# Kernel optimization log

Measured on AMD Instinct MI355X. Metric: run time of the kernel, lower is better.

Reference implementation:

```python
import jax, jax.numpy as jnp
import numpy as np

NUM_BITS = 10
MEM_SIZE = 2 ** NUM_BITS  # 1024
HIDDEN = 1024
INPUT = 1024
BATCH = 16384
LN_EPS = 1e-5


def setup_inputs() -> dict:
    key = jax.random.key(0)
    ks = jax.random.split(key, 8)
    s = 0.02
    return {
        "x": jax.random.normal(ks[0], (BATCH, INPUT), jnp.float32),
        "h_prev": jax.random.normal(ks[1], (BATCH, HIDDEN), jnp.float32),
        "memory": jax.random.normal(ks[2], (MEM_SIZE, HIDDEN), jnp.float32),
        "W_w": jax.random.normal(ks[3], (HIDDEN, INPUT), jnp.float32) * s,
        "W_b": jnp.zeros((HIDDEN,), jnp.float32),
        "U_w": jax.random.normal(ks[4], (HIDDEN, HIDDEN), jnp.float32) * s,
        "U_b": jnp.zeros((HIDDEN,), jnp.float32),
        "Q_w": jax.random.normal(ks[5], (HIDDEN, HIDDEN), jnp.float32) * s,
        "Q_b": jnp.zeros((HIDDEN,), jnp.float32),
        "M_w": jax.random.normal(ks[6], (NUM_BITS, HIDDEN), jnp.float32) * s,
        "M_b": jnp.zeros((NUM_BITS,), jnp.float32),
        "ln_g": jnp.ones((HIDDEN,), jnp.float32),
        "ln_b": jnp.zeros((HIDDEN,), jnp.float32),
    }


def reference(x, h_prev, memory, W_w, W_b, U_w, U_b, Q_w, Q_b, M_w, M_b, ln_g, ln_b):
    # Binary address from h_prev (eval-mode hard threshold, non-differentiable)
    powers = jnp.asarray(2 ** np.arange(NUM_BITS - 1, -1, -1), dtype=x.dtype)  # [num_bits]
    logits = h_prev @ M_w.T + M_b                              # [B, num_bits]
    binary = (jax.nn.sigmoid(logits) > 0.5).astype(x.dtype)    # hard bits
    index = jnp.clip((binary * powers).sum(-1).astype(jnp.int32), 0, MEM_SIZE - 1)  # [B]
    h_mem = memory[index]                                      # gather [B, H]
    # Fused linear combine + LayerNorm + sigmoid
    pre = x @ W_w.T + W_b + h_prev @ U_w.T + U_b + h_mem @ Q_w.T + Q_b  # [B, H]
    mu = pre.mean(-1, keepdims=True)
    var = ((pre - mu) ** 2).mean(-1, keepdims=True)            # biased var (torch LN)
    norm = (pre - mu) * jax.lax.rsqrt(var + LN_EPS)
    return jax.nn.sigmoid(norm * ln_g + ln_b)                  # h_new [B, H]
```

## Files before the change

### kernel.cpp

```cpp
#include <hip/hip_runtime.h>

#define BATCH   16384
#define HIDDEN  1024
#define K2      2048
#define MEMSZ   1024
#define NBITS   10

#define BM 256
#define BN 256
#define BK 64
#define NT (K2 / BK)

#define U_BM    262144
#define U_TOT   2359296
#define SBLK    2304
#define SSTRIDE (SBLK * 256)

typedef __bf16 bf16x8 __attribute__((ext_vector_type(8)));
typedef float  f32x4  __attribute__((ext_vector_type(4)));
typedef unsigned short u16x8 __attribute__((ext_vector_type(8)));

__device__ __forceinline__ unsigned short f2bf(float f) {
    unsigned int u = __float_as_uint(f);
    u += 0x7FFFu + ((u >> 16) & 1u);
    return (unsigned short)(u >> 16);
}

__device__ __forceinline__ float bf2f(unsigned short u) {
    return __uint_as_float((unsigned int)u << 16);
}

__device__ __forceinline__ u16x8 f2bf8(float4 a, float4 b) {
    u16x8 r;
    r[0] = f2bf(a.x); r[1] = f2bf(a.y); r[2] = f2bf(a.z); r[3] = f2bf(a.w);
    r[4] = f2bf(b.x); r[5] = f2bf(b.y); r[6] = f2bf(b.z); r[7] = f2bf(b.w);
    return r;
}

__device__ __forceinline__ ushort4 f2bf4(float4 a) {
    ushort4 r;
    r.x = f2bf(a.x); r.y = f2bf(a.y); r.z = f2bf(a.z); r.w = f2bf(a.w);
    return r;
}

__device__ __forceinline__ void gload_lds16(const void* g, void* l) {
    __builtin_amdgcn_global_load_lds(
        (const __attribute__((address_space(1))) unsigned int*)g,
        (__attribute__((address_space(3))) unsigned int*)l,
        16, 0, 0);
}

__global__ __launch_bounds__(256) void stream_kernel(
        const float* __restrict__ W, const float* __restrict__ U,
        const float* __restrict__ x,
        unsigned short* __restrict__ Bm, unsigned short* __restrict__ A) {
    const int u0 = blockIdx.x * 256 + threadIdx.x;
    const float* s4[4];
    unsigned short* d4[4];
#pragma unroll
    for (int i = 0; i < 4; ++i) {
        int u = u0 + i * SSTRIDE;
        if (u < U_BM) {
            int n  = u >> 8;
            int k8 = (u & 255) << 3;
            s4[i] = (k8 < 1024) ? (W + (size_t)n * 1024 + k8)
                                : (U + (size_t)n * 1024 + (k8 - 1024));
            d4[i] = Bm + (size_t)n * K2 + k8;
        } else {
            int e = (u - U_BM) << 3;
            int row = e >> 10, col = e & 1023;
            s4[i] = x + (size_t)row * HIDDEN + col;
            d4[i] = A + (size_t)row * K2 + col;
        }
    }
    float4 va[4], vb[4];
#pragma unroll
    for (int i = 0; i < 4; ++i) {
        va[i] = *reinterpret_cast<const float4*>(s4[i]);
        vb[i] = *reinterpret_cast<const float4*>(s4[i] + 4);
    }
    __builtin_amdgcn_sched_barrier(0);
#pragma unroll
    for (int i = 0; i < 4; ++i)
        *reinterpret_cast<u16x8*>(d4[i]) = f2bf8(va[i], vb[i]);
}

__global__ __launch_bounds__(256) void build_kernel(
        const float* __restrict__ h_prev,
        const float* __restrict__ M_w, const float* __restrict__ M_b,
        unsigned short* __restrict__ A, int* __restrict__ idxbuf) {
    __shared__ float mw[NBITS * HIDDEN];
    for (int i = threadIdx.x; i < (NBITS * HIDDEN) / 4; i += 256)
        reinterpret_cast<float4*>(mw)[i] = reinterpret_cast<const float4*>(M_w)[i];
    __syncthreads();

    const int wv   = threadIdx.x >> 6;
    const int lane = threadIdx.x & 63;
    const int row0 = (blockIdx.x * 4 + wv) * 2;
    const int c4   = lane * 4;

    float4 h[2][4];
#pragma unroll
    for (int r = 0; r < 2; ++r) {
        const float* hr = h_prev + (size_t)(row0 + r) * HIDDEN;
#pragma unroll
        for (int seg = 0; seg < 4; ++seg)
            h[r][seg] = *reinterpret_cast<const float4*>(hr + seg * 256 + c4);
    }

    float s[2][NBITS];
#pragma unroll
    for (int j = 0; j < NBITS; ++j) {
        const float* mj = mw + j * HIDDEN;
        float4 m[4];
#pragma unroll
        for (int seg = 0; seg < 4; ++seg)
            m[seg] = *reinterpret_cast<const float4*>(mj + seg * 256 + c4);
#pragma unroll
        for (int r = 0; r < 2; ++r) {
            float acc = 0.f;
#pragma unroll
            for (int seg = 0; seg < 4; ++seg)
                acc += h[r][seg].x * m[seg].x + h[r][seg].y * m[seg].y
                     + h[r][seg].z * m[seg].z + h[r][seg].w * m[seg].w;
            s[r][j] = acc;
        }
    }
#pragma unroll
    for (int off = 32; off >= 1; off >>= 1) {
#pragma unroll
        for (int r = 0; r < 2; ++r)
#pragma unroll
            for (int j = 0; j < NBITS; ++j)
                s[r][j] += __shfl_xor(s[r][j], off, 64);
    }
#pragma unroll
    for (int r = 0; r < 2; ++r) {
        int idx = 0;
#pragma unroll
        for (int j = 0; j < NBITS; ++j)
            if (s[r][j] + M_b[j] > 0.f) idx |= 1 << (NBITS - 1 - j);
        if (lane == 0) idxbuf[row0 + r] = idx;
    }

#pragma unroll
    for (int r = 0; r < 2; ++r) {
        unsigned short* arow = A + (size_t)(row0 + r) * K2 + 1024;
#pragma unroll
        for (int seg = 0; seg < 4; ++seg)
            *reinterpret_cast<ushort4*>(arow + seg * 256 + c4) = f2bf4(h[r][seg]);
    }
}

__global__ __launch_bounds__(256) void mq_kernel(
        const float* __restrict__ memory,
        const float* __restrict__ Q,
        float* __restrict__ MQ) {
    __shared__ unsigned short As[128 * 32];
    __shared__ unsigned short Bs[128 * 32];

    const int mb = blockIdx.x >> 3;
    const int nb = blockIdx.x & 7;
    const int t    = threadIdx.x;
    const int lane = t & 63;
    const int w    = t >> 6;
    const int wr   = w >> 1, wc = w & 1;
    const int rr   = lane & 15, rq = lane >> 4;
    const int srow = t >> 1;
    const int scol = (t & 1) * 16;
    const int swr  = (srow & 3) << 4;

    f32x4 acc[4][4] = {};

    for (int kt = 0; kt < 32; ++kt) {
        const int k0 = kt * 32;
        const float* ap = memory + (size_t)(mb * 128 + srow) * 1024 + k0 + scol;
        const float* bp = Q      + (size_t)(nb * 128 + srow) * 1024 + k0 + scol;
        float4 a0 = *reinterpret_cast<const float4*>(ap);
        float4 a1 = *reinterpret_cast<const float4*>(ap + 4);
        float4 a2 = *reinterpret_cast<const float4*>(ap + 8);
        float4 a3 = *reinterpret_cast<const float4*>(ap + 12);
        float4 b0 = *reinterpret_cast<const float4*>(bp);
        float4 b1 = *reinterpret_cast<const float4*>(bp + 4);
        float4 b2 = *reinterpret_cast<const float4*>(bp + 8);
        float4 b3 = *reinterpret_cast<const float4*>(bp + 12);
        __syncthreads();
        {
            char* ar = reinterpret_cast<char*>(As) + srow * 64;
            char* br = reinterpret_cast<char*>(Bs) + srow * 64;
            *reinterpret_cast<u16x8*>(ar + ((scol * 2)      ^ swr)) = f2bf8(a0, a1);
            *reinterpret_cast<u16x8*>(ar + ((scol * 2 + 16) ^ swr)) = f2bf8(a2, a3);
            *reinterpret_cast<u16x8*>(br + ((scol * 2)      ^ swr)) = f2bf8(b0, b1);
            *reinterpret_cast<u16x8*>(br + ((scol * 2 + 16) ^ swr)) = f2bf8(b2, b3);
        }
        __syncthreads();
        bf16x8 af[4], bfv[4];
#pragma unroll
        for (int m = 0; m < 4; ++m) {
            int r = wr * 64 + m * 16 + rr;
            af[m] = *reinterpret_cast<const bf16x8*>(
                reinterpret_cast<const char*>(As) + r * 64 + ((rq * 16) ^ ((r & 3) << 4)));
        }
#pragma unroll
        for (int n = 0; n < 4; ++n) {
            int r = wc * 64 + n * 16 + rr;
            bfv[n] = *reinterpret_cast<const bf16x8*>(
                reinterpret_cast<const char*>(Bs) + r * 64 + ((rq * 16) ^ ((r & 3) << 4)));
        }
#pragma unroll
        for (int m = 0; m < 4; ++m)
#pragma unroll
            for (int n = 0; n < 4; ++n)
                acc[m][n] = __builtin_amdgcn_mfma_f32_16x16x32_bf16(
                    af[m], bfv[n], acc[m][n], 0, 0, 0);
    }

#pragma unroll
    for (int m = 0; m < 4; ++m)
#pragma unroll
        for (int n = 0; n < 4; ++n) {
            int gcol = nb * 128 + wc * 64 + n * 16 + rr;
#pragma unroll
            for (int j = 0; j < 4; ++j) {
                int grow = mb * 128 + wr * 64 + m * 16 + rq * 4 + j;
                MQ[(size_t)grow * 1024 + gcol] = acc[m][n][j];
            }
        }
}


__device__ __forceinline__ void stage_g(const unsigned short* __restrict__ src,
                                        int rowbase, int kt, int g,
                                        unsigned short* ldsTile, int t) {
    const int o      = g * 8192 + t * 16;
    const int row    = o >> 7;
    const int inner  = o & 127;
    const int sinner = inner ^ ((row & 7) << 4);
    const char* gp = reinterpret_cast<const char*>(
                         src + (size_t)(rowbase + row) * K2 + kt * BK) + sinner;
    gload_lds16(gp, reinterpret_cast<char*>(ldsTile) + o);
}

__device__ __forceinline__ bf16x8 ldsfrag(const unsigned short* tile, int row,
                                          int kbyte_x_sw) {
    return *reinterpret_cast<const bf16x8*>(
        reinterpret_cast<const char*>(tile) + row * 128 + kbyte_x_sw);
}

#define PH_BAR()                                                     \
    do {                                                             \
        asm volatile("" ::: "memory");                               \
        __builtin_amdgcn_s_barrier();                                \
        asm volatile("" ::: "memory");                               \
    } while (0)

#define LGKM(N)                                                      \
    do {                                                             \
        asm volatile("s_waitcnt lgkmcnt(" #N ")" ::: "memory");      \
        __builtin_amdgcn_sched_barrier(0);                           \
    } while (0)

#define MFMA_Q(AF, BF, MB, NB)                                                 \
    {                                                                          \
        __builtin_amdgcn_s_setprio(1);                                         \
        _Pragma("unroll") for (int m_ = 0; m_ < 4; ++m_)                       \
        _Pragma("unroll") for (int n_ = 0; n_ < 2; ++n_)                       \
        _Pragma("unroll") for (int kk_ = 0; kk_ < 2; ++kk_)                    \
            acc[(MB) + m_][(NB) + n_] =                                        \
                __builtin_amdgcn_mfma_f32_16x16x32_bf16(                       \
                    AF[m_][kk_], BF[n_][kk_],                                  \
                    acc[(MB) + m_][(NB) + n_], 0, 0, 0);                       \
        __builtin_amdgcn_s_setprio(0);                                         \
    }

template <bool BF16C>
__global__ __launch_bounds__(512, 2) void gemm_kernel(
        const unsigned short* __restrict__ A,
        const unsigned short* __restrict__ Bm,
        void* __restrict__ Cout) {
    __shared__ alignas(16) unsigned short lds[2][2][BM * BK];

    const int bid  = blockIdx.x;
    const int wgid = (bid & 7) * 32 + (bid >> 3);
    const int mblk = wgid >> 2;
    const int nblk = wgid & 3;

    const int t    = threadIdx.x;
    const int lane = t & 63;
    const int w    = t >> 6;
    const int wr   = w >> 2;
    const int wc   = w & 3;
    const int rr   = lane & 15;
    const int rq   = lane >> 4;
    const int sw   = (rr & 7) << 4;
    const int rqb  = rq * 16;
    const int wrb  = wr * 128;
    const int wcb  = wc * 64;

    const int arow = mblk * BM;
    const int brow = nblk * BN;

    f32x4 acc[8][4] = {};

    {
#pragma unroll
        for (int g = 0; g < 4; ++g) stage_g(A,  arow, 0, g, &lds[0][0][0], t);
#pragma unroll
        for (int g = 0; g < 4; ++g) stage_g(Bm, brow, 0, g, &lds[0][1][0], t);
#pragma unroll
        for (int g = 0; g < 4; ++g) stage_g(Bm, brow, 1, g, &lds[1][1][0], t);
#pragma unroll
        for (int g = 0; g < 4; ++g) stage_g(A,  arow, 1, g, &lds[1][0][0], t);
        asm volatile("s_waitcnt vmcnt(8)" ::: "memory");
        asm volatile("" ::: "memory");
        __builtin_amdgcn_s_barrier();
    }

    bf16x8 af  [4][2];
    bf16x8 af2 [4][2];
    bf16x8 bfr01[2][2];
    bf16x8 bfr23[2][2];

#pragma unroll
    for (int m = 0; m < 4; ++m) {
        af[m][0] = ldsfrag(&lds[0][0][0], wrb + m * 16 + rr, (rqb) ^ sw);
        af[m][1] = ldsfrag(&lds[0][0][0], wrb + m * 16 + rr, (64 + rqb) ^ sw);
    }
#pragma unroll
    for (int n = 0; n < 2; ++n) {
        bfr01[n][0] = ldsfrag(&lds[0][1][0], wcb + n * 16 + rr, (rqb) ^ sw);
        bfr01[n][1] = ldsfrag(&lds[0][1][0], wcb + n * 16 + rr, (64 + rqb) ^ sw);
    }

    for (int kt = 0; kt < NT; ++kt) {
        const int c = kt & 1;
        const unsigned short* At  = &lds[c][0][0];
        const unsigned short* Bt  = &lds[c][1][0];
        const unsigned short* nxA = &lds[c ^ 1][0][0];
        const unsigned short* nxB = &lds[c ^ 1][1][0];
        unsigned short* curA = &lds[c][0][0];
        unsigned short* curB = &lds[c][1][0];
        const bool pf1 = (kt + 1 < NT);
        const bool pf2 = (kt + 2 < NT);

        PH_BAR();
#pragma unroll
        for (int n = 0; n < 2; ++n) {
            bfr23[n][0] = ldsfrag(Bt, wcb + 32 + n * 16 + rr, (rqb) ^ sw);
            bfr23[n][1] = ldsfrag(Bt, wcb + 32 + n * 16 + rr, (64 + rqb) ^ sw);
        }
        af2[0][0] = ldsfrag(At, wrb + 64 + rr, (rqb) ^ sw);
        af2[0][1] = ldsfrag(At, wrb + 64 + rr, (64 + rqb) ^ sw);
        LGKM(6);
        MFMA_Q(af, bfr01, 0, 0);

        PH_BAR();
#pragma unroll
        for (int m = 1; m < 4; ++m) {
            af2[m][0] = ldsfrag(At, wrb + 64 + m * 16 + rr, (rqb) ^ sw);
            af2[m][1] = ldsfrag(At, wrb + 64 + m * 16 + rr, (64 + rqb) ^ sw);
        }
        LGKM(8);
        MFMA_Q(af, bfr23, 0, 2);
        __builtin_amdgcn_sched_barrier(0);
        asm volatile("s_waitcnt vmcnt(0)" ::: "memory");
        asm volatile("" ::: "memory");

        PH_BAR();
        if (pf2) {
            stage_g(Bm, brow, kt + 2, 0, curB, t);
            stage_g(Bm, brow, kt + 2, 1, curB, t);
            stage_g(Bm, brow, kt + 2, 2, curB, t);
            stage_g(Bm, brow, kt + 2, 3, curB, t);
        }
        if (pf1) {
#pragma unroll
            for (int m = 0; m < 3; ++m) {
                af[m][0] = ldsfrag(nxA, wrb + m * 16 + rr, (rqb) ^ sw);
                af[m][1] = ldsfrag(nxA, wrb + m * 16 + rr, (64 + rqb) ^ sw);
            }
            LGKM(6);
        } else {
            LGKM(0);
        }
        MFMA_Q(af2, bfr01, 4, 0);

        PH_BAR();
        if (pf2) {
            stage_g(A, arow, kt + 2, 0, curA, t);
            stage_g(A, arow, kt + 2, 1, curA, t);
            stage_g(A, arow, kt + 2, 2, curA, t);
            stage_g(A, arow, kt + 2, 3, curA, t);
        }
        if (pf1) {
            af[3][0] = ldsfrag(nxA, wrb + 48 + rr, (rqb) ^ sw);
            af[3][1] = ldsfrag(nxA, wrb + 48 + rr, (64 + rqb) ^ sw);
#pragma unroll
            for (int n = 0; n < 2; ++n) {
                bfr01[n][0] = ldsfrag(nxB, wcb + n * 16 + rr, (rqb) ^ sw);
                bfr01[n][1] = ldsfrag(nxB, wcb + n * 16 + rr, (64 + rqb) ^ sw);
            }
        }
        MFMA_Q(af2, bfr23, 4, 2);
    }

#pragma unroll
    for (int mi = 0; mi < 8; ++mi) {
#pragma unroll
        for (int n = 0; n < 4; ++n) {
            const int gcol = nblk * BN + wcb + n * 16 + rr;
#pragma unroll
            for (int j = 0; j < 4; ++j) {
                const int grow = mblk * BM + wrb + mi * 16 + rq * 4 + j;
                if constexpr (BF16C) {
                    ((unsigned short*)Cout)[(size_t)grow * HIDDEN + gcol] =
                        f2bf(acc[mi][n][j]);
                } else {
                    ((float*)Cout)[(size_t)grow * HIDDEN + gcol] = acc[mi][n][j];
                }
            }
        }
    }
}

template <bool BF16C>
__global__ __launch_bounds__(256) void ln_kernel(
        const void* __restrict__ Cin, float* __restrict__ out,
        const int* __restrict__ idxbuf,
        const float* __restrict__ MQ,
        const float* __restrict__ W_b, const float* __restrict__ U_b,
        const float* __restrict__ Q_b, const float* __restrict__ ln_g,
        const float* __restrict__ ln_b) {
    const int row = blockIdx.x;
    const int t   = threadIdx.x;
    const int midx = idxbuf[row];
    const float4* mqp = reinterpret_cast<const float4*>(MQ + (size_t)midx * HIDDEN);

    float4 p;
    if constexpr (BF16C) {
        ushort4 uv = reinterpret_cast<const ushort4*>(
            (const unsigned short*)Cin + (size_t)row * HIDDEN)[t];
        p.x = bf2f(uv.x); p.y = bf2f(uv.y); p.z = bf2f(uv.z); p.w = bf2f(uv.w);
    } else {
        p = reinterpret_cast<const float4*>(
            (const float*)Cin + (size_t)row * HIDDEN)[t];
    }
    float4 mq = mqp[t];
    float4 bw = reinterpret_cast<const float4*>(W_b)[t];
    float4 bu = reinterpret_cast<const float4*>(U_b)[t];
    float4 bq = reinterpret_cast<const float4*>(Q_b)[t];
    p.x += mq.x + bw.x + bu.x + bq.x;
    p.y += mq.y + bw.y + bu.y + bq.y;
    p.z += mq.z + bw.z + bu.z + bq.z;
    p.w += mq.w + bw.w + bu.w + bq.w;

    float s  = p.x + p.y + p.z + p.w;
    float sq = p.x * p.x + p.y * p.y + p.z * p.z + p.w * p.w;
#pragma unroll
    for (int off = 32; off >= 1; off >>= 1) {
        s  += __shfl_xor(s,  off, 64);
        sq += __shfl_xor(sq, off, 64);
    }
    __shared__ float red[8];
    const int lane = t & 63, w = t >> 6;
    if (lane == 0) { red[w] = s; red[4 + w] = sq; }
    __syncthreads();
    const float S    = red[0] + red[1] + red[2] + red[3];
    const float SQ   = red[4] + red[5] + red[6] + red[7];
    const float mean = S * (1.0f / HIDDEN);
    const float var  = SQ * (1.0f / HIDDEN) - mean * mean;
    const float rstd = rsqrtf(var + 1e-5f);

    float4 g = reinterpret_cast<const float4*>(ln_g)[t];
    float4 b = reinterpret_cast<const float4*>(ln_b)[t];
    float4 o;
    o.x = 1.f / (1.f + __expf(-((p.x - mean) * rstd * g.x + b.x)));
    o.y = 1.f / (1.f + __expf(-((p.y - mean) * rstd * g.y + b.y)));
    o.z = 1.f / (1.f + __expf(-((p.z - mean) * rstd * g.z + b.z)));
    o.w = 1.f / (1.f + __expf(-((p.w - mean) * rstd * g.w + b.w)));
    reinterpret_cast<float4*>(out + (size_t)row * HIDDEN)[t] = o;
}

extern "C" void kernel_launch(void* const* d_in, const int* in_sizes, int n_in,
                              void* d_out, int out_size, void* d_ws, size_t ws_size,
                              hipStream_t stream) {
    const float* x      = (const float*)d_in[0];
    const float* h_prev = (const float*)d_in[1];
    const float* memory = (const float*)d_in[2];
    const float* W_w    = (const float*)d_in[3];
    const float* W_b    = (const float*)d_in[4];
    const float* U_w    = (const float*)d_in[5];
    const float* U_b    = (const float*)d_in[6];
    const float* Q_w    = (const float*)d_in[7];
    const float* Q_b    = (const float*)d_in[8];
    const float* M_w    = (const float*)d_in[9];
    const float* M_b    = (const float*)d_in[10];
    const float* ln_g   = (const float*)d_in[11];
    const float* ln_b   = (const float*)d_in[12];

    char* ws = (char*)d_ws;
    unsigned short* A   = (unsigned short*)(ws);
    unsigned short* Bm  = (unsigned short*)(ws + 67108864);
    float*          MQ  = (float*)         (ws + 71303168);
    int*            idx = (int*)           (ws + 75497472);
    unsigned short* Cb  = (unsigned short*)(ws + 75563008);
    const bool bf16c = ws_size >= (size_t)75563008 + 33554432;

    float* pre = (float*)d_out;

    hipLaunchKernelGGL(stream_kernel, dim3(SBLK), dim3(256), 0, stream,
                       W_w, U_w, x, Bm, A);
    hipLaunchKernelGGL(build_kernel, dim3(BATCH / 8), dim3(256), 0, stream,
                       h_prev, M_w, M_b, A, idx);
    hipLaunchKernelGGL(mq_kernel, dim3(64), dim3(256), 0, stream,
                       memory, Q_w, MQ);
    if (bf16c) {
        hipLaunchKernelGGL((gemm_kernel<true>), dim3((BATCH / BM) * (HIDDEN / BN)),
                           dim3(512), 0, stream, A, Bm, (void*)Cb);
        hipLaunchKernelGGL((ln_kernel<true>), dim3(BATCH), dim3(256), 0, stream,
                           (const void*)Cb, (float*)d_out, idx, MQ,
                           W_b, U_b, Q_b, ln_g, ln_b);
    } else {
        hipLaunchKernelGGL((gemm_kernel<false>), dim3((BATCH / BM) * (HIDDEN / BN)),
                           dim3(512), 0, stream, A, Bm, (void*)pre);
        hipLaunchKernelGGL((ln_kernel<false>), dim3(BATCH), dim3(256), 0, stream,
                           (const void*)pre, (float*)d_out, idx, MQ,
                           W_b, U_b, Q_b, ln_g, ln_b);
    }
}
```

Baseline: 187.1 us.

## Merge front-end kernels into one launch and drop bf16 intermediate path

```diff
diff --git a/kernel.cpp b/kernel.cpp
--- a/kernel.cpp
+++ b/kernel.cpp
@@ -11,10 +11,12 @@
 #define BK 64
 #define NT (K2 / BK)
 
+#define MQB     64
 #define U_BM    262144
 #define U_TOT   2359296
 #define SBLK    2304
 #define SSTRIDE (SBLK * 256)
+#define BBLK    (BATCH / 8)
 
 typedef __bf16 bf16x8 __attribute__((ext_vector_type(8)));
 typedef float  f32x4  __attribute__((ext_vector_type(4)));
@@ -24,10 +26,6 @@
     unsigned int u = __float_as_uint(f);
     u += 0x7FFFu + ((u >> 16) & 1u);
     return (unsigned short)(u >> 16);
-}
-
-__device__ __forceinline__ float bf2f(unsigned short u) {
-    return __uint_as_float((unsigned int)u << 16);
 }
 
 __device__ __forceinline__ u16x8 f2bf8(float4 a, float4 b) {
@@ -50,53 +48,130 @@
         16, 0, 0);
 }
 
-__global__ __launch_bounds__(256) void stream_kernel(
+__global__ __launch_bounds__(256) void front_kernel(
         const float* __restrict__ W, const float* __restrict__ U,
-        const float* __restrict__ x,
-        unsigned short* __restrict__ Bm, unsigned short* __restrict__ A) {
-    const int u0 = blockIdx.x * 256 + threadIdx.x;
-    const float* s4[4];
-    unsigned short* d4[4];
-#pragma unroll
-    for (int i = 0; i < 4; ++i) {
-        int u = u0 + i * SSTRIDE;
-        if (u < U_BM) {
-            int n  = u >> 8;
-            int k8 = (u & 255) << 3;
-            s4[i] = (k8 < 1024) ? (W + (size_t)n * 1024 + k8)
-                                : (U + (size_t)n * 1024 + (k8 - 1024));
-            d4[i] = Bm + (size_t)n * K2 + k8;
-        } else {
-            int e = (u - U_BM) << 3;
-            int row = e >> 10, col = e & 1023;
-            s4[i] = x + (size_t)row * HIDDEN + col;
-            d4[i] = A + (size_t)row * K2 + col;
-        }
-    }
-    float4 va[4], vb[4];
-#pragma unroll
-    for (int i = 0; i < 4; ++i) {
-        va[i] = *reinterpret_cast<const float4*>(s4[i]);
-        vb[i] = *reinterpret_cast<const float4*>(s4[i] + 4);
-    }
-    __builtin_amdgcn_sched_barrier(0);
-#pragma unroll
-    for (int i = 0; i < 4; ++i)
-        *reinterpret_cast<u16x8*>(d4[i]) = f2bf8(va[i], vb[i]);
-}
-
-__global__ __launch_bounds__(256) void build_kernel(
-        const float* __restrict__ h_prev,
+        const float* __restrict__ x, const float* __restrict__ h_prev,
+        const float* __restrict__ memory, const float* __restrict__ Q,
         const float* __restrict__ M_w, const float* __restrict__ M_b,
-        unsigned short* __restrict__ A, int* __restrict__ idxbuf) {
-    __shared__ float mw[NBITS * HIDDEN];
+        unsigned short* __restrict__ Bm, unsigned short* __restrict__ A,
+        float* __restrict__ MQ, int* __restrict__ idxbuf) {
+    __shared__ alignas(16) char shmem[40960];
+
+    if (blockIdx.x < MQB) {
+        unsigned short* As = reinterpret_cast<unsigned short*>(shmem);
+        unsigned short* Bs = reinterpret_cast<unsigned short*>(shmem + 8192);
+
+        const int mb = blockIdx.x >> 3;
+        const int nb = blockIdx.x & 7;
+        const int t    = threadIdx.x;
+        const int lane = t & 63;
+        const int w    = t >> 6;
+        const int wr   = w >> 1, wc = w & 1;
+        const int rr   = lane & 15, rq = lane >> 4;
+        const int srow = t >> 1;
+        const int scol = (t & 1) * 16;
+        const int swr  = (srow & 3) << 4;
+
+        f32x4 acc[4][4] = {};
+
+        for (int kt = 0; kt < 32; ++kt) {
+            const int k0 = kt * 32;
+            const float* ap = memory + (size_t)(mb * 128 + srow) * 1024 + k0 + scol;
+            const float* bp = Q      + (size_t)(nb * 128 + srow) * 1024 + k0 + scol;
+            float4 a0 = *reinterpret_cast<const float4*>(ap);
+            float4 a1 = *reinterpret_cast<const float4*>(ap + 4);
+            float4 a2 = *reinterpret_cast<const float4*>(ap + 8);
+            float4 a3 = *reinterpret_cast<const float4*>(ap + 12);
+            float4 b0 = *reinterpret_cast<const float4*>(bp);
+            float4 b1 = *reinterpret_cast<const float4*>(bp + 4);
+            float4 b2 = *reinterpret_cast<const float4*>(bp + 8);
+            float4 b3 = *reinterpret_cast<const float4*>(bp + 12);
+            __syncthreads();
+            {
+                char* ar = reinterpret_cast<char*>(As) + srow * 64;
+                char* br = reinterpret_cast<char*>(Bs) + srow * 64;
+                *reinterpret_cast<u16x8*>(ar + ((scol * 2)      ^ swr)) = f2bf8(a0, a1);
+                *reinterpret_cast<u16x8*>(ar + ((scol * 2 + 16) ^ swr)) = f2bf8(a2, a3);
+                *reinterpret_cast<u16x8*>(br + ((scol * 2)      ^ swr)) = f2bf8(b0, b1);
+                *reinterpret_cast<u16x8*>(br + ((scol * 2 + 16) ^ swr)) = f2bf8(b2, b3);
+            }
+            __syncthreads();
+            bf16x8 af[4], bfv[4];
+#pragma unroll
+            for (int m = 0; m < 4; ++m) {
+                int r = wr * 64 + m * 16 + rr;
+                af[m] = *reinterpret_cast<const bf16x8*>(
+                    reinterpret_cast<const char*>(As) + r * 64 + ((rq * 16) ^ ((r & 3) << 4)));
+            }
+#pragma unroll
+            for (int n = 0; n < 4; ++n) {
+                int r = wc * 64 + n * 16 + rr;
+                bfv[n] = *reinterpret_cast<const bf16x8*>(
+                    reinterpret_cast<const char*>(Bs) + r * 64 + ((rq * 16) ^ ((r & 3) << 4)));
+            }
+#pragma unroll
+            for (int m = 0; m < 4; ++m)
+#pragma unroll
+                for (int n = 0; n < 4; ++n)
+                    acc[m][n] = __builtin_amdgcn_mfma_f32_16x16x32_bf16(
+                        af[m], bfv[n], acc[m][n], 0, 0, 0);
+        }
+
+#pragma unroll
+        for (int m = 0; m < 4; ++m)
+#pragma unroll
+            for (int n = 0; n < 4; ++n) {
+                int gcol = nb * 128 + wc * 64 + n * 16 + rr;
+#pragma unroll
+                for (int j = 0; j < 4; ++j) {
+                    int grow = mb * 128 + wr * 64 + m * 16 + rq * 4 + j;
+                    MQ[(size_t)grow * 1024 + gcol] = acc[m][n][j];
+                }
+            }
+        return;
+    }
+
+    if (blockIdx.x < MQB + SBLK) {
+        const int u0 = (blockIdx.x - MQB) * 256 + threadIdx.x;
+        const float* s4[4];
+        unsigned short* d4[4];
+#pragma unroll
+        for (int i = 0; i < 4; ++i) {
+            int u = u0 + i * SSTRIDE;
+            if (u < U_BM) {
+                int n  = u >> 8;
+                int k8 = (u & 255) << 3;
+                s4[i] = (k8 < 1024) ? (W + (size_t)n * 1024 + k8)
+                                    : (U + (size_t)n * 1024 + (k8 - 1024));
+                d4[i] = Bm + (size_t)n * K2 + k8;
+            } else {
+                int e = (u - U_BM) << 3;
+                int row = e >> 10, col = e & 1023;
+                s4[i] = x + (size_t)row * HIDDEN + col;
+                d4[i] = A + (size_t)row * K2 + col;
+            }
+        }
+        float4 va[4], vb[4];
+#pragma unroll
+        for (int i = 0; i < 4; ++i) {
+            va[i] = *reinterpret_cast<const float4*>(s4[i]);
+            vb[i] = *reinterpret_cast<const float4*>(s4[i] + 4);
+        }
+        __builtin_amdgcn_sched_barrier(0);
+#pragma unroll
+        for (int i = 0; i < 4; ++i)
+            *reinterpret_cast<u16x8*>(d4[i]) = f2bf8(va[i], vb[i]);
+        return;
+    }
+
+    float* mw = reinterpret_cast<float*>(shmem);
     for (int i = threadIdx.x; i < (NBITS * HIDDEN) / 4; i += 256)
         reinterpret_cast<float4*>(mw)[i] = reinterpret_cast<const float4*>(M_w)[i];
     __syncthreads();
 
     const int wv   = threadIdx.x >> 6;
     const int lane = threadIdx.x & 63;
-    const int row0 = (blockIdx.x * 4 + wv) * 2;
+    const int row0 = ((blockIdx.x - MQB - SBLK) * 4 + wv) * 2;
     const int c4   = lane * 4;
 
     float4 h[2][4];
@@ -150,82 +225,6 @@
         for (int seg = 0; seg < 4; ++seg)
             *reinterpret_cast<ushort4*>(arow + seg * 256 + c4) = f2bf4(h[r][seg]);
     }
-}
-
-__global__ __launch_bounds__(256) void mq_kernel(
-        const float* __restrict__ memory,
-        const float* __restrict__ Q,
-        float* __restrict__ MQ) {
-    __shared__ unsigned short As[128 * 32];
-    __shared__ unsigned short Bs[128 * 32];
-
-    const int mb = blockIdx.x >> 3;
-    const int nb = blockIdx.x & 7;
-    const int t    = threadIdx.x;
-    const int lane = t & 63;
-    const int w    = t >> 6;
-    const int wr   = w >> 1, wc = w & 1;
-    const int rr   = lane & 15, rq = lane >> 4;
-    const int srow = t >> 1;
-    const int scol = (t & 1) * 16;
-    const int swr  = (srow & 3) << 4;
-
-    f32x4 acc[4][4] = {};
-
-    for (int kt = 0; kt < 32; ++kt) {
-        const int k0 = kt * 32;
-        const float* ap = memory + (size_t)(mb * 128 + srow) * 1024 + k0 + scol;
-        const float* bp = Q      + (size_t)(nb * 128 + srow) * 1024 + k0 + scol;
-        float4 a0 = *reinterpret_cast<const float4*>(ap);
-        float4 a1 = *reinterpret_cast<const float4*>(ap + 4);
-        float4 a2 = *reinterpret_cast<const float4*>(ap + 8);
-        float4 a3 = *reinterpret_cast<const float4*>(ap + 12);
-        float4 b0 = *reinterpret_cast<const float4*>(bp);
-        float4 b1 = *reinterpret_cast<const float4*>(bp + 4);
-        float4 b2 = *reinterpret_cast<const float4*>(bp + 8);
-        float4 b3 = *reinterpret_cast<const float4*>(bp + 12);
-        __syncthreads();
-        {
-            char* ar = reinterpret_cast<char*>(As) + srow * 64;
-            char* br = reinterpret_cast<char*>(Bs) + srow * 64;
-            *reinterpret_cast<u16x8*>(ar + ((scol * 2)      ^ swr)) = f2bf8(a0, a1);
-            *reinterpret_cast<u16x8*>(ar + ((scol * 2 + 16) ^ swr)) = f2bf8(a2, a3);
-            *reinterpret_cast<u16x8*>(br + ((scol * 2)      ^ swr)) = f2bf8(b0, b1);
-            *reinterpret_cast<u16x8*>(br + ((scol * 2 + 16) ^ swr)) = f2bf8(b2, b3);
-        }
-        __syncthreads();
-        bf16x8 af[4], bfv[4];
-#pragma unroll
-        for (int m = 0; m < 4; ++m) {
-            int r = wr * 64 + m * 16 + rr;
-            af[m] = *reinterpret_cast<const bf16x8*>(
-                reinterpret_cast<const char*>(As) + r * 64 + ((rq * 16) ^ ((r & 3) << 4)));
-        }
-#pragma unroll
-        for (int n = 0; n < 4; ++n) {
-            int r = wc * 64 + n * 16 + rr;
-            bfv[n] = *reinterpret_cast<const bf16x8*>(
-                reinterpret_cast<const char*>(Bs) + r * 64 + ((rq * 16) ^ ((r & 3) << 4)));
-        }
-#pragma unroll
-        for (int m = 0; m < 4; ++m)
-#pragma unroll
-            for (int n = 0; n < 4; ++n)
-                acc[m][n] = __builtin_amdgcn_mfma_f32_16x16x32_bf16(
-                    af[m], bfv[n], acc[m][n], 0, 0, 0);
-    }
-
-#pragma unroll
-    for (int m = 0; m < 4; ++m)
-#pragma unroll
-        for (int n = 0; n < 4; ++n) {
-            int gcol = nb * 128 + wc * 64 + n * 16 + rr;
-#pragma unroll
-            for (int j = 0; j < 4; ++j) {
-                int grow = mb * 128 + wr * 64 + m * 16 + rq * 4 + j;
-                MQ[(size_t)grow * 1024 + gcol] = acc[m][n][j];
-            }
-        }
 }
 
 
@@ -273,11 +272,10 @@
         __builtin_amdgcn_s_setprio(0);                                         \
     }
 
-template <bool BF16C>
 __global__ __launch_bounds__(512, 2) void gemm_kernel(
         const unsigned short* __restrict__ A,
         const unsigned short* __restrict__ Bm,
-        void* __restrict__ Cout) {
+        float* __restrict__ C) {
     __shared__ alignas(16) unsigned short lds[2][2][BM * BK];
 
     const int bid  = blockIdx.x;
@@ -412,20 +410,14 @@
 #pragma unroll
             for (int j = 0; j < 4; ++j) {
                 const int grow = mblk * BM + wrb + mi * 16 + rq * 4 + j;
-                if constexpr (BF16C) {
-                    ((unsigned short*)Cout)[(size_t)grow * HIDDEN + gcol] =
-                        f2bf(acc[mi][n][j]);
-                } else {
-                    ((float*)Cout)[(size_t)grow * HIDDEN + gcol] = acc[mi][n][j];
-                }
-            }
-        }
-    }
-}
-
-template <bool BF16C>
+                C[(size_t)grow * HIDDEN + gcol] = acc[mi][n][j];
+            }
+        }
+    }
+}
+
 __global__ __launch_bounds__(256) void ln_kernel(
-        const void* __restrict__ Cin, float* __restrict__ out,
+        float* __restrict__ C,
         const int* __restrict__ idxbuf,
         const float* __restrict__ MQ,
         const float* __restrict__ W_b, const float* __restrict__ U_b,
@@ -434,17 +426,10 @@
     const int row = blockIdx.x;
     const int t   = threadIdx.x;
     const int midx = idxbuf[row];
+    float4* rowp = reinterpret_cast<float4*>(C + (size_t)row * HIDDEN);
     const float4* mqp = reinterpret_cast<const float4*>(MQ + (size_t)midx * HIDDEN);
 
-    float4 p;
-    if constexpr (BF16C) {
-        ushort4 uv = reinterpret_cast<const ushort4*>(
-            (const unsigned short*)Cin + (size_t)row * HIDDEN)[t];
-        p.x = bf2f(uv.x); p.y = bf2f(uv.y); p.z = bf2f(uv.z); p.w = bf2f(uv.w);
-    } else {
-        p = reinterpret_cast<const float4*>(
-            (const float*)Cin + (size_t)row * HIDDEN)[t];
-    }
+    float4 p  = rowp[t];
     float4 mq = mqp[t];
     float4 bw = reinterpret_cast<const float4*>(W_b)[t];
     float4 bu = reinterpret_cast<const float4*>(U_b)[t];
@@ -478,7 +463,7 @@
     o.y = 1.f / (1.f + __expf(-((p.y - mean) * rstd * g.y + b.y)));
     o.z = 1.f / (1.f + __expf(-((p.z - mean) * rstd * g.z + b.z)));
     o.w = 1.f / (1.f + __expf(-((p.w - mean) * rstd * g.w + b.w)));
-    reinterpret_cast<float4*>(out + (size_t)row * HIDDEN)[t] = o;
+    rowp[t] = o;
 }
 
 extern "C" void kernel_launch(void* const* d_in, const int* in_sizes, int n_in,
@@ -503,28 +488,14 @@
     unsigned short* Bm  = (unsigned short*)(ws + 67108864);
     float*          MQ  = (float*)         (ws + 71303168);
     int*            idx = (int*)           (ws + 75497472);
-    unsigned short* Cb  = (unsigned short*)(ws + 75563008);
-    const bool bf16c = ws_size >= (size_t)75563008 + 33554432;
 
     float* pre = (float*)d_out;
 
-    hipLaunchKernelGGL(stream_kernel, dim3(SBLK), dim3(256), 0, stream,
-                       W_w, U_w, x, Bm, A);
-    hipLaunchKernelGGL(build_kernel, dim3(BATCH / 8), dim3(256), 0, stream,
-                       h_prev, M_w, M_b, A, idx);
-    hipLaunchKernelGGL(mq_kernel, dim3(64), dim3(256), 0, stream,
-                       memory, Q_w, MQ);
-    if (bf16c) {
-        hipLaunchKernelGGL((gemm_kernel<true>), dim3((BATCH / BM) * (HIDDEN / BN)),
-                           dim3(512), 0, stream, A, Bm, (void*)Cb);
-        hipLaunchKernelGGL((ln_kernel<true>), dim3(BATCH), dim3(256), 0, stream,
-                           (const void*)Cb, (float*)d_out, idx, MQ,
-                           W_b, U_b, Q_b, ln_g, ln_b);
-    } else {
-        hipLaunchKernelGGL((gemm_kernel<false>), dim3((BATCH / BM) * (HIDDEN / BN)),
-                           dim3(512), 0, stream, A, Bm, (void*)pre);
-        hipLaunchKernelGGL((ln_kernel<false>), dim3(BATCH), dim3(256), 0, stream,
-                           (const void*)pre, (float*)d_out, idx, MQ,
-                           W_b, U_b, Q_b, ln_g, ln_b);
-    }
-}
+    hipLaunchKernelGGL(front_kernel, dim3(MQB + SBLK + BBLK), dim3(256), 0, stream,
+                       W_w, U_w, x, h_prev, memory, Q_w, M_w, M_b,
+                       Bm, A, MQ, idx);
+    hipLaunchKernelGGL(gemm_kernel, dim3((BATCH / BM) * (HIDDEN / BN)), dim3(512), 0, stream,
+                       A, Bm, pre);
+    hipLaunchKernelGGL(ln_kernel, dim3(BATCH), dim3(256), 0, stream,
+                       pre, idx, MQ, W_b, U_b, Q_b, ln_g, ln_b);
+}
```

Result: faster. 164.2 us (-12.2%).
